# Optimization experiments

Hardware: AMD Instinct MI355X
Metric: run time of the kernel (lower is better)

Reference implementation:

```python
import jax, jax.numpy as jnp
import numpy as np

B, S, D = 1, 2048, 2048
NH, NKV, HD = 16, 8, 128
FF = 8192
L = 2
V = 32000
THETA = 10000.0
EPS = 1e-5
SCALE = 0.02


def setup_inputs() -> dict:
    key = jax.random.key(0)
    ks = jax.random.split(key, 16)
    return {
        "input_ids": jax.random.randint(ks[0], (B, S), 0, V, dtype=jnp.int32),
        "embed": jax.random.normal(ks[1], (V, D), jnp.float32) * SCALE,
        "Wq": jax.random.normal(ks[2], (L, D, NH * HD), jnp.float32) * SCALE,
        "Wk": jax.random.normal(ks[3], (L, D, NKV * HD), jnp.float32) * SCALE,
        "Wv": jax.random.normal(ks[4], (L, D, NKV * HD), jnp.float32) * SCALE,
        "Wo": jax.random.normal(ks[5], (L, NH * HD, D), jnp.float32) * SCALE,
        "Wgate": jax.random.normal(ks[6], (L, D, FF), jnp.float32) * SCALE,
        "Wup": jax.random.normal(ks[7], (L, D, FF), jnp.float32) * SCALE,
        "Wdown": jax.random.normal(ks[8], (L, FF, D), jnp.float32) * SCALE,
        "norm_attn": jnp.ones((L, D), jnp.float32),
        "norm_mlp": jnp.ones((L, D), jnp.float32),
        "norm_final": jnp.ones((D,), jnp.float32),
        "lm_head": jax.random.normal(ks[9], (D, V), jnp.float32) * SCALE,
        "D1": jax.random.normal(ks[10], (S,), jnp.float32) + 2.0,
        "D2": jax.random.normal(ks[11], (HD,), jnp.float32) + 2.0,
        "D3": jax.random.normal(ks[12], (S,), jnp.float32) + 2.0,
    }


def _rms_norm(x, w):
    return x * jax.lax.rsqrt(jnp.mean(x * x, axis=-1, keepdims=True) + EPS) * w


def _rotate_half(x):
    x1, x2 = jnp.split(x, 2, axis=-1)
    return jnp.concatenate([-x2, x1], axis=-1)


def _forward(input_ids, embed, Wq, Wk, Wv, Wo, Wgate, Wup, Wdown,
             norm_attn, norm_mlp, norm_final, lm_head, D1, D2, D3):
    # RoPE tables: [1,1,S,HD]
    inv_freq = 1.0 / (THETA ** (jnp.arange(0, HD, 2, dtype=jnp.float32) / HD))
    freqs = jnp.arange(S, dtype=jnp.float32)[:, None] * inv_freq[None, :]
    emb = jnp.concatenate([freqs, freqs], axis=-1)
    cos = jnp.cos(emb)[None, None]
    sin = jnp.sin(emb)[None, None]
    causal = jnp.tril(jnp.ones((S, S), dtype=bool))
    neg = jnp.finfo(jnp.float32).min
    D1i, D2i, D3i = 1.0 / D1, 1.0 / D2, 1.0 / D3
    n_rep = NH // NKV

    h = embed[input_ids]  # [B,S,D]
    for l in range(L):
        # --- attention block ---
        x = _rms_norm(h, norm_attn[l])
        q = (x @ Wq[l]).reshape(B, S, NH, HD).transpose(0, 2, 1, 3)   # [B,NH,S,HD]
        k = (x @ Wk[l]).reshape(B, S, NKV, HD).transpose(0, 2, 1, 3)  # [B,NKV,S,HD]
        v = (x @ Wv[l]).reshape(B, S, NKV, HD).transpose(0, 2, 1, 3)
        q = q * cos + _rotate_half(q) * sin
        k = k * cos + _rotate_half(k) * sin
        # repeat_kv (GQA)
        k = jnp.repeat(k, n_rep, axis=1)
        v = jnp.repeat(v, n_rep, axis=1)
        # TEE diagonal encryption: Q' = D1 Q D2, K'^T = D2^-1 K^T D3
        q_enc = q * D1[None, None, :, None] * D2[None, None, None, :]
        k_enc = k * D3[None, None, :, None] * D2i[None, None, None, :]
        scores = jnp.einsum('bhqd,bhkd->bhqk', q_enc, k_enc)
        # decrypt: D1^-1 (Q'K'^T) D3^-1  (mathematically cancels encryption)
        scores = scores * D1i[None, None, :, None] * D3i[None, None, None, :]
        scores = scores / jnp.sqrt(jnp.float32(HD))
        scores = jnp.where(causal[None, None], scores, neg)
        probs = jax.nn.softmax(scores, axis=-1)
        o = jnp.einsum('bhqk,bhkd->bhqd', probs, v)
        o = o.transpose(0, 2, 1, 3).reshape(B, S, NH * HD)
        h = h + o @ Wo[l]
        # --- SwiGLU MLP block ---
        x = _rms_norm(h, norm_mlp[l])
        h = h + (jax.nn.silu(x @ Wgate[l]) * (x @ Wup[l])) @ Wdown[l]

    h = _rms_norm(h, norm_final)
    return h @ lm_head  # logits [B,S,V]


def reference(input_ids, embed, Wq, Wk, Wv, Wo, Wgate, Wup, Wdown,
              norm_attn, norm_mlp, norm_final, lm_head, D1, D2, D3):
    return _forward(input_ids, embed, Wq, Wk, Wv, Wo, Wgate, Wup, Wdown,
                    norm_attn, norm_mlp, norm_final, lm_head, D1, D2, D3)
```

## Files before the change

### kernel.cpp

```cpp
#include <hip/hip_runtime.h>
#include <cstdint>
#include <cstddef>

typedef __attribute__((ext_vector_type(4))) float f32x4;
typedef __attribute__((ext_vector_type(8))) short short8;
typedef __attribute__((ext_vector_type(4))) unsigned int u32x4;

static const int TS = 2048;
static const int DM = 2048;
static const int NHEAD = 16, NKVH = 8, HDIM = 128;
static const int FFD = 8192;
static const int NVOC = 32000;
static const int QKVN = 4096;

__device__ __forceinline__ unsigned short f2bf(float f){
  unsigned int u = __builtin_bit_cast(unsigned int, f);
  u += 0x7FFFu + ((u >> 16) & 1u);
  return (unsigned short)(u >> 16);
}
__device__ __forceinline__ float bf2f(short h){
  unsigned int u = ((unsigned int)(unsigned short)h) << 16;
  return __builtin_bit_cast(float, u);
}
__device__ __forceinline__ f32x4 mfma16(short8 a, short8 b, f32x4 c){
  return __builtin_amdgcn_mfma_f32_16x16x32_bf16(a, b, c, 0, 0, 0);
}
__device__ __forceinline__ void gload16(const void* g, void* l){
  __builtin_amdgcn_global_load_lds(
      (const __attribute__((address_space(1))) unsigned int*)g,
      (__attribute__((address_space(3))) unsigned int*)l, 16, 0, 0);
}
__device__ __forceinline__ long toff(int r, int k, int ldk){
  return ((long)((r >> 4) * ldk + (k >> 5)) << 9)
       + (((k & 31) >> 3) << 7) + ((r & 15) << 3) + (k & 7);
}

__global__ void rope_tables_k(float* __restrict__ cosT, float* __restrict__ sinT){
  int idx = blockIdx.x * 256 + threadIdx.x;
  int s = idx >> 6, j = idx & 63;
  float inv = exp2f(-(float)j * (13.287712379549449f / 64.0f));
  float ang = (float)s * inv;
  cosT[idx] = cosf(ang);
  sinT[idx] = sinf(ang);
}

__global__ void embed_k(const int* __restrict__ ids, const float* __restrict__ E,
                        float* __restrict__ h){
  int s = blockIdx.x, tid = threadIdx.x;
  long id = ids[s];
  const f32x4* src = (const f32x4*)(E + id * (long)DM);
  f32x4* dst = (f32x4*)(h + (long)s * DM);
  dst[tid] = src[tid];
  dst[tid + 256] = src[tid + 256];
}

__global__ void rmsnorm_k(const float* __restrict__ x, const float* __restrict__ w,
                          short* __restrict__ out){
  int s = blockIdx.x, tid = threadIdx.x;
  const float* row = x + (long)s * DM;
  f32x4 v0 = *(const f32x4*)&row[tid * 8];
  f32x4 v1 = *(const f32x4*)&row[tid * 8 + 4];
  float ss = v0[0]*v0[0] + v0[1]*v0[1] + v0[2]*v0[2] + v0[3]*v0[3]
           + v1[0]*v1[0] + v1[1]*v1[1] + v1[2]*v1[2] + v1[3]*v1[3];
  #pragma unroll
  for (int off = 32; off; off >>= 1) ss += __shfl_xor(ss, off);
  __shared__ float sred[4];
  int wave = tid >> 6, lane = tid & 63;
  if (lane == 0) sred[wave] = ss;
  __syncthreads();
  float tot = sred[0] + sred[1] + sred[2] + sred[3];
  float r = rsqrtf(tot * (1.0f / (float)DM) + 1e-5f);
  f32x4 w0 = *(const f32x4*)&w[tid * 8];
  f32x4 w1 = *(const f32x4*)&w[tid * 8 + 4];
  short8 o;
  #pragma unroll
  for (int j = 0; j < 4; j++) o[j] = (short)f2bf(v0[j] * r * w0[j]);
  #pragma unroll
  for (int j = 0; j < 4; j++) o[4 + j] = (short)f2bf(v1[j] * r * w1[j]);
  *(short8*)&out[toff(s, tid * 8, DM >> 5)] = o;
}

__global__ void transpose_k(const float* __restrict__ B, short* __restrict__ Bt,
                            int K, int N){
  __shared__ float t[64][65];
  int tid = threadIdx.x;
  int kb = blockIdx.y * 64, nb = blockIdx.x * 64;
  int r0 = tid >> 4, c4 = tid & 15;
  const int ldk = K >> 5;
  #pragma unroll
  for (int p = 0; p < 4; p++){
    int r = r0 + p * 16;
    f32x4 v = *(const f32x4*)&B[(long)(kb + r) * N + nb + c4 * 4];
    t[r][c4*4+0] = v[0]; t[r][c4*4+1] = v[1]; t[r][c4*4+2] = v[2]; t[r][c4*4+3] = v[3];
  }
  __syncthreads();
  int n0 = tid >> 3, k0 = (tid & 7) * 8;
  #pragma unroll
  for (int p = 0; p < 2; p++){
    int n = n0 + p * 32;
    short8 o;
    #pragma unroll
    for (int j = 0; j < 8; j++) o[j] = (short)f2bf(t[k0 + j][n]);
    *(short8*)&Bt[toff(nb + n, kb + k0, ldk)] = o;
  }
}

__global__ void vtrans_k(const short* __restrict__ vb, short* __restrict__ vtb, int stride){
  int s0 = blockIdx.x * 64, kv = blockIdx.y;
  int tid = threadIdx.x;
  int s = s0 + (tid & 63);
  int d0 = (tid >> 6) * 8;
  #pragma unroll
  for (int p = 0; p < 4; p++){
    int d = d0 + p * 32;
    short8 v = *(const short8*)&vb[(long)s * stride + kv * HDIM + d];
    #pragma unroll
    for (int j = 0; j < 8; j++)
      vtb[(long)(kv * HDIM + d + j) * TS + s] = v[j];
  }
}

__global__ void rope_apply_k(short* __restrict__ buf, const float* __restrict__ cosT,
                             const float* __restrict__ sinT, int nh, int stride, int coloff){
  int idx = blockIdx.x * 256 + threadIdx.x;
  int j = idx & 63;
  int t = idx >> 6;
  int hh = t % nh;
  int s = t / nh;
  long base = (long)s * stride + coloff + hh * HDIM + j;
  float c = cosT[s * 64 + j], sn = sinT[s * 64 + j];
  float x1 = bf2f(buf[base]), x2 = bf2f(buf[base + 64]);
  buf[base]      = (short)f2bf(x1 * c - x2 * sn);
  buf[base + 64] = (short)f2bf(x2 * c + x1 * sn);
}

__global__ void reduce4_k(const float* __restrict__ p, float* __restrict__ h){
  const long stride = (long)TS * DM;
  long i = ((long)blockIdx.x * 256 + threadIdx.x) * 4;
  f32x4 a = *(const f32x4*)&h[i];
  f32x4 v0 = *(const f32x4*)&p[i];
  f32x4 v1 = *(const f32x4*)&p[i + stride];
  f32x4 v2 = *(const f32x4*)&p[i + 2 * stride];
  f32x4 v3 = *(const f32x4*)&p[i + 3 * stride];
  a = a + ((v0 + v1) + (v2 + v3));
  *(f32x4*)&h[i] = a;
}

template<int EPI>
__global__ __launch_bounds__(512, 2)
void gemm256(const short* __restrict__ A, int ldkA,
             const short* __restrict__ Bt, int ldkB,
             float* __restrict__ Cf, short* __restrict__ Cb,
             const short* __restrict__ Xtra, int N, int K, int ldkC){
  __shared__ short lds[4][2][8192];
  const int tid = threadIdx.x;
  const int wid = tid >> 6, lane = tid & 63;
  const int wr = wid >> 2, wc = wid & 3;
  const int fr = lane & 15, fch = lane >> 4;
  const int nt = K >> 5;

  const int z = blockIdx.y;
  const int k0 = z * nt;

  const int nbt = N >> 8;
  const int nwg = nbt << 3;
  const int q = nwg >> 3;
  const int swz = (blockIdx.x & 7) * q + (blockIdx.x >> 3);
  const int mb = swz & 7, nb = swz >> 3;

  const short* Abase = A  + ((long)(mb * 16) * ldkA + k0) * 512 + lane * 8;
  const short* Bbase = Bt + ((long)(nb * 16) * ldkB + k0) * 512 + lane * 8;
  const int gA0 = wid * 2, gA1 = wid * 2 + 1;

  short8 aE[4], aO[4], bE[2], bO[2];
  f32x4 acc[8][4] = {};

#define STG_A(bufc, g_, tau_) \
  gload16(Abase + ((long)(g_) * ldkA + (tau_)) * 512, &lds[bufc][0][(g_) * 512])
#define STG_B(bufc, g_, tau_) \
  gload16(Bbase + ((long)(g_) * ldkB + (tau_)) * 512, &lds[bufc][1][(g_) * 512])
#define RDA(dst, bufc, mh) do{ \
    _Pragma("unroll") \
    for (int j_ = 0; j_ < 4; j_++) \
      dst[j_] = *(const short8*)&lds[bufc][0][(wr * 8 + (mh) * 4 + j_) * 512 + fch * 128 + fr * 8]; \
  }while(0)
#define RDB(dst, bufc, nh) do{ \
    _Pragma("unroll") \
    for (int i_ = 0; i_ < 2; i_++) \
      dst[i_] = *(const short8*)&lds[bufc][1][(wc * 4 + (nh) * 2 + i_) * 512 + fch * 128 + fr * 8]; \
  }while(0)
#define MM8(va, vb, mh, nh) do{ \
    __builtin_amdgcn_s_setprio(1); \
    _Pragma("unroll") \
    for (int j_ = 0; j_ < 4; j_++) \
      _Pragma("unroll") \
      for (int i_ = 0; i_ < 2; i_++) \
        acc[(mh)*4+j_][(nh)*2+i_] = mfma16(va[j_], vb[i_], acc[(mh)*4+j_][(nh)*2+i_]); \
    __builtin_amdgcn_s_setprio(0); \
  }while(0)
#define SB __builtin_amdgcn_sched_barrier(0)

#define TILE(t_, bufR, bufN, bufS, bC, bNx) do{ \
    const int tau_ = ((t_) + 3 < nt) ? (t_) + 3 : nt - 1; \
    RDB(bNx, bufR, 1); STG_A(bufS, gA0, tau_); SB; MM8(aE, bC, 0, 0); \
    RDA(aO,  bufR, 1); STG_A(bufS, gA1, tau_); SB; MM8(aE, bNx, 0, 1); \
    asm volatile("s_waitcnt vmcnt(6)" ::: "memory"); \
    __builtin_amdgcn_s_barrier(); \
    RDA(aE,  bufN, 0); STG_B(bufS, gA0, tau_); SB; MM8(aO, bNx, 1, 1); \
    RDB(bNx, bufN, 0); STG_B(bufS, gA1, tau_); SB; MM8(aO, bC, 1, 0); \
    __builtin_amdgcn_s_barrier(); \
  }while(0)

  STG_A(0, gA0, 0); STG_A(0, gA1, 0); STG_B(0, gA0, 0); STG_B(0, gA1, 0);
  STG_A(1, gA0, 1); STG_A(1, gA1, 1); STG_B(1, gA0, 1); STG_B(1, gA1, 1);
  STG_A(2, gA0, 2); STG_A(2, gA1, 2); STG_B(2, gA0, 2); STG_B(2, gA1, 2);
  asm volatile("s_waitcnt vmcnt(8)" ::: "memory");
  __builtin_amdgcn_s_barrier();
  RDA(aE, 0, 0); RDB(bE, 0, 0);

  const int nIter = nt >> 2;
  for (int it = 0; it < nIter; ++it){
    const int t0 = it << 2;
    TILE(t0 + 0, 0, 1, 3, bE, bO);
    TILE(t0 + 1, 1, 2, 0, bO, bE);
    TILE(t0 + 2, 2, 3, 1, bE, bO);
    TILE(t0 + 3, 3, 0, 2, bO, bE);
  }
  asm volatile("s_waitcnt vmcnt(0)" ::: "memory");

#undef STG_A
#undef STG_B
#undef RDA
#undef RDB
#undef MM8
#undef SB
#undef TILE

  const int rb0 = mb * 256 + wr * 128 + fch * 4;
  const int cb0 = nb * 256 + wc * 64 + fr;
  const long pbase = (EPI == 5) ? (long)z * ((long)TS * N) : 0;
  #pragma unroll
  for (int m = 0; m < 8; m++)
    #pragma unroll
    for (int n = 0; n < 4; n++)
      #pragma unroll
      for (int i = 0; i < 4; i++){
        const int rr = rb0 + m * 16 + i, cc = cb0 + n * 16;
        long idx = (long)rr * N + cc;
        float v = acc[m][n][i];
        if constexpr (EPI == 0) Cf[idx] = v;
        else if constexpr (EPI == 1) Cb[idx] = (short)f2bf(v);
        else if constexpr (EPI == 3){
          float sg = 1.0f / (1.0f + __expf(-v));
          Cb[idx] = (short)f2bf(v * sg);
        } else if constexpr (EPI == 4){
          float g = bf2f(Xtra[idx]);
          Cb[toff(rr, cc, ldkC)] = (short)f2bf(g * v);
        } else {
          Cf[pbase + idx] = v;
        }
      }
}

__device__ __forceinline__ int qoff(int r, int cB){ return r * 256 + (cB ^ ((r & 7) << 4)); }
__device__ __forceinline__ int voff(int d, int cB){ return d * 128 + (cB ^ ((d & 7) << 4)); }
__device__ __forceinline__ int poff(int r, int cB){ return r * 128 + (cB ^ ((r & 7) << 4)); }

__global__ __launch_bounds__(256)
void attn_k(const short* __restrict__ qb, const short* __restrict__ kb,
            const short* __restrict__ vtb, short* __restrict__ ob){
  __shared__ short Qs[64 * 128];
  __shared__ short Ks[64 * 128];
  __shared__ short Vt[128 * 64];
  __shared__ short Ps[64 * 64];
  const int tid = threadIdx.x, wave = tid >> 6, lane = tid & 63;
  const int qt = blockIdx.x, head = blockIdx.y, kvh = head >> 1;
  const float scale = 0.08838834764831845f;

  {
    int r0 = tid >> 4, c16 = tid & 15;
    #pragma unroll
    for (int p = 0; p < 4; p++){
      int r = r0 + p * 16;
      u32x4 v = *(const u32x4*)&qb[(long)(qt * 64 + r) * QKVN + head * HDIM + c16 * 8];
      *(u32x4*)((char*)Qs + qoff(r, c16 * 16)) = v;
    }
  }

  float mrun[4] = {-1e30f, -1e30f, -1e30f, -1e30f};
  float lrun[4] = {0.f, 0.f, 0.f, 0.f};
  f32x4 accO[8] = {};

  for (int kt = 0; kt <= qt; kt++){
    __syncthreads();
    {
      int r0 = tid >> 4, c16 = tid & 15;
      #pragma unroll
      for (int p = 0; p < 4; p++){
        int r = r0 + p * 16;
        u32x4 v = *(const u32x4*)&kb[(long)(kt * 64 + r) * QKVN + kvh * HDIM + c16 * 8];
        *(u32x4*)((char*)Ks + qoff(r, c16 * 16)) = v;
      }
      int vr0 = tid >> 3, vc = tid & 7;
      #pragma unroll
      for (int p = 0; p < 4; p++){
        int d = vr0 + p * 32;
        u32x4 v = *(const u32x4*)&vtb[(long)(kvh * HDIM + d) * TS + kt * 64 + vc * 8];
        *(u32x4*)((char*)Vt + voff(d, vc * 16)) = v;
      }
    }
    __syncthreads();

    f32x4 sacc[4] = {};
    #pragma unroll
    for (int k4 = 0; k4 < 4; k4++){
      short8 aq = *(const short8*)((const char*)Qs +
                   qoff(wave * 16 + (lane & 15), k4 * 64 + (lane >> 4) * 16));
      #pragma unroll
      for (int n = 0; n < 4; n++){
        short8 bk = *(const short8*)((const char*)Ks +
                     qoff(n * 16 + (lane & 15), k4 * 64 + (lane >> 4) * 16));
        sacc[n] = mfma16(aq, bk, sacc[n]);
      }
    }

    const bool diag = (kt == qt);
    float mt[4] = {-1e30f, -1e30f, -1e30f, -1e30f};
    #pragma unroll
    for (int n = 0; n < 4; n++)
      #pragma unroll
      for (int i = 0; i < 4; i++){
        float v = sacc[n][i] * scale;
        if (diag){
          int rr = (lane >> 4) * 4 + i + wave * 16;
          int cc = n * 16 + (lane & 15);
          if (cc > rr) v = -1e30f;
        }
        sacc[n][i] = v;
        mt[i] = fmaxf(mt[i], v);
      }
    #pragma unroll
    for (int off = 1; off < 16; off <<= 1)
      #pragma unroll
      for (int i = 0; i < 4; i++) mt[i] = fmaxf(mt[i], __shfl_xor(mt[i], off));
    float alpha[4], rsum[4];
    #pragma unroll
    for (int i = 0; i < 4; i++){
      float mn = fmaxf(mrun[i], mt[i]);
      alpha[i] = __expf(mrun[i] - mn);
      mrun[i] = mn;
      rsum[i] = 0.f;
    }
    #pragma unroll
    for (int n = 0; n < 4; n++)
      #pragma unroll
      for (int i = 0; i < 4; i++){
        float p = __expf(sacc[n][i] - mrun[i]);
        sacc[n][i] = p;
        rsum[i] += p;
      }
    #pragma unroll
    for (int off = 1; off < 16; off <<= 1)
      #pragma unroll
      for (int i = 0; i < 4; i++) rsum[i] += __shfl_xor(rsum[i], off);
    #pragma unroll
    for (int i = 0; i < 4; i++) lrun[i] = lrun[i] * alpha[i] + rsum[i];

    #pragma unroll
    for (int n = 0; n < 4; n++)
      #pragma unroll
      for (int i = 0; i < 4; i++){
        int rr = wave * 16 + (lane >> 4) * 4 + i;
        int cc = n * 16 + (lane & 15);
        *(short*)((char*)Ps + poff(rr, cc * 2)) = (short)f2bf(sacc[n][i]);
      }

    #pragma unroll
    for (int n = 0; n < 8; n++)
      #pragma unroll
      for (int i = 0; i < 4; i++) accO[n][i] *= alpha[i];
    #pragma unroll
    for (int ks = 0; ks < 2; ks++){
      short8 ap = *(const short8*)((const char*)Ps +
                   poff(wave * 16 + (lane & 15), ks * 64 + (lane >> 4) * 16));
      #pragma unroll
      for (int n = 0; n < 8; n++){
        short8 bv = *(const short8*)((const char*)Vt +
                     voff(n * 16 + (lane & 15), ks * 64 + (lane >> 4) * 16));
        accO[n] = mfma16(ap, bv, accO[n]);
      }
    }
  }

  #pragma unroll
  for (int i = 0; i < 4; i++){
    float inv = 1.0f / lrun[i];
    int rr = qt * 64 + wave * 16 + (lane >> 4) * 4 + i;
    #pragma unroll
    for (int n = 0; n < 8; n++){
      int cc = head * HDIM + n * 16 + (lane & 15);
      ob[toff(rr, cc, DM >> 5)] = (short)f2bf(accO[n][i] * inv);
    }
  }
}

extern "C" void kernel_launch(void* const* d_in, const int* in_sizes, int n_in,
                              void* d_out, int out_size, void* d_ws, size_t ws_size,
                              hipStream_t stream){
  (void)in_sizes; (void)n_in; (void)out_size; (void)ws_size;
  const int*   ids = (const int*)d_in[0];
  const float* E   = (const float*)d_in[1];
  const float* Wq  = (const float*)d_in[2];
  const float* Wk  = (const float*)d_in[3];
  const float* Wv  = (const float*)d_in[4];
  const float* Wo  = (const float*)d_in[5];
  const float* Wg  = (const float*)d_in[6];
  const float* Wu  = (const float*)d_in[7];
  const float* Wd  = (const float*)d_in[8];
  const float* nA  = (const float*)d_in[9];
  const float* nM  = (const float*)d_in[10];
  const float* nF  = (const float*)d_in[11];
  const float* LMH = (const float*)d_in[12];
  float* out = (float*)d_out;

  char* ws = (char*)d_ws;
  size_t off = 0;
  auto alloc = [&](size_t bytes){ void* p = ws + off; off += (bytes + 255) & ~(size_t)255; return p; };
  float* h    = (float*)alloc((size_t)TS * DM * 4);
  short* xb   = (short*)alloc((size_t)TS * DM * 2);
  short* qkvb = (short*)alloc((size_t)TS * QKVN * 2);
  short* vtb  = (short*)alloc((size_t)NKVH * HDIM * TS * 2);
  short* obuf = (short*)alloc((size_t)TS * DM * 2);
  short* sg   = (short*)alloc((size_t)TS * FFD * 2);
  short* actb = (short*)alloc((size_t)TS * FFD * 2);
  float* cosT = (float*)alloc((size_t)TS * 64 * 4);
  float* sinT = (float*)alloc((size_t)TS * 64 * 4);
  short* wT   = (short*)alloc((size_t)NVOC * DM * 2);
  float* pPart = (float*)((char*)wT + (size_t)36 * 1024 * 1024);

  rope_tables_k<<<512, 256, 0, stream>>>(cosT, sinT);
  embed_k<<<TS, 256, 0, stream>>>(ids, E, h);

  for (int l = 0; l < 2; l++){
    rmsnorm_k<<<TS, 256, 0, stream>>>(h, nA + (size_t)l * DM, xb);
    transpose_k<<<dim3(32, 32), 256, 0, stream>>>(Wq + (size_t)l * DM * DM, wT, DM, DM);
    transpose_k<<<dim3(16, 32), 256, 0, stream>>>(Wk + (size_t)l * DM * 1024, wT + (size_t)2048 * DM, DM, 1024);
    transpose_k<<<dim3(16, 32), 256, 0, stream>>>(Wv + (size_t)l * DM * 1024, wT + (size_t)3072 * DM, DM, 1024);
    gemm256<1><<<dim3(128), 512, 0, stream>>>(xb, 64, wT, 64, nullptr, qkvb, nullptr, QKVN, DM, 0);
    rope_apply_k<<<8192, 256, 0, stream>>>(qkvb, cosT, sinT, NHEAD, QKVN, 0);
    rope_apply_k<<<4096, 256, 0, stream>>>(qkvb, cosT, sinT, NKVH, QKVN, 2048);
    vtrans_k<<<dim3(32, 8), 256, 0, stream>>>(qkvb + 3072, vtb, QKVN);
    attn_k<<<dim3(32, 16), 256, 0, stream>>>(qkvb, qkvb + 2048, vtb, obuf);
    transpose_k<<<dim3(32, 32), 256, 0, stream>>>(Wo + (size_t)l * DM * DM, wT, DM, DM);
    gemm256<5><<<dim3(64, 4), 512, 0, stream>>>(obuf, 64, wT, 64, pPart, nullptr, nullptr, DM, DM / 4, 0);
    reduce4_k<<<4096, 256, 0, stream>>>(pPart, h);
    rmsnorm_k<<<TS, 256, 0, stream>>>(h, nM + (size_t)l * DM, xb);
    transpose_k<<<dim3(128, 32), 256, 0, stream>>>(Wg + (size_t)l * DM * FFD, wT, DM, FFD);
    gemm256<3><<<dim3(256), 512, 0, stream>>>(xb, 64, wT, 64, nullptr, sg, nullptr, FFD, DM, 0);
    transpose_k<<<dim3(128, 32), 256, 0, stream>>>(Wu + (size_t)l * DM * FFD, wT, DM, FFD);
    gemm256<4><<<dim3(256), 512, 0, stream>>>(xb, 64, wT, 64, nullptr, actb, sg, FFD, DM, FFD >> 5);
    transpose_k<<<dim3(32, 128), 256, 0, stream>>>(Wd + (size_t)l * FFD * DM, wT, FFD, DM);
    gemm256<5><<<dim3(64, 4), 512, 0, stream>>>(actb, 256, wT, 256, pPart, nullptr, nullptr, DM, FFD / 4, 0);
    reduce4_k<<<4096, 256, 0, stream>>>(pPart, h);
  }

  rmsnorm_k<<<TS, 256, 0, stream>>>(h, nF, xb);
  transpose_k<<<dim3(500, 32), 256, 0, stream>>>(LMH, wT, DM, NVOC);
  gemm256<0><<<dim3(1000), 512, 0, stream>>>(xb, 64, wT, 64, out, nullptr, nullptr, NVOC, DM, 0);
}
```

Measured before the change: 1.359 ms.

## Fuse split-K reduction with RMSNorm and add double-buffered GEMM for LM head

Replaces the separate split-K partial reduction and following RMSNorm launches with one reduce_rms kernel that adds the partials into the residual and immediately normalizes to bf16. This drops one full pass over the residual stream per block. It also adds a new GEMM variant with two LDS buffers instead of four, using launch bounds for higher occupancy, and uses it for the large LM-head projection. The smaller LDS footprint trades pipeline depth for more resident workgroups.

```diff
diff --git a/kernel.cpp b/kernel.cpp
--- a/kernel.cpp
+++ b/kernel.cpp
@@ -77,6 +77,49 @@
   for (int j = 0; j < 4; j++) o[j] = (short)f2bf(v0[j] * r * w0[j]);
   #pragma unroll
   for (int j = 0; j < 4; j++) o[4 + j] = (short)f2bf(v1[j] * r * w1[j]);
+  *(short8*)&out[toff(s, tid * 8, DM >> 5)] = o;
+}
+
+__global__ void reduce_rms_k(const float* __restrict__ p, float* __restrict__ h,
+                             const float* __restrict__ w, short* __restrict__ out){
+  const long stride = (long)TS * DM;
+  int s = blockIdx.x, tid = threadIdx.x;
+  long i = (long)s * DM + tid * 8;
+  f32x4 a0 = *(const f32x4*)&h[i];
+  f32x4 a1 = *(const f32x4*)&h[i + 4];
+  {
+    f32x4 v0 = *(const f32x4*)&p[i];
+    f32x4 v1 = *(const f32x4*)&p[i + stride];
+    f32x4 v2 = *(const f32x4*)&p[i + 2 * stride];
+    f32x4 v3 = *(const f32x4*)&p[i + 3 * stride];
+    a0 = a0 + ((v0 + v1) + (v2 + v3));
+  }
+  {
+    f32x4 v0 = *(const f32x4*)&p[i + 4];
+    f32x4 v1 = *(const f32x4*)&p[i + 4 + stride];
+    f32x4 v2 = *(const f32x4*)&p[i + 4 + 2 * stride];
+    f32x4 v3 = *(const f32x4*)&p[i + 4 + 3 * stride];
+    a1 = a1 + ((v0 + v1) + (v2 + v3));
+  }
+  *(f32x4*)&h[i] = a0;
+  *(f32x4*)&h[i + 4] = a1;
+  float ss = a0[0]*a0[0] + a0[1]*a0[1] + a0[2]*a0[2] + a0[3]*a0[3]
+           + a1[0]*a1[0] + a1[1]*a1[1] + a1[2]*a1[2] + a1[3]*a1[3];
+  #pragma unroll
+  for (int off = 32; off; off >>= 1) ss += __shfl_xor(ss, off);
+  __shared__ float sred[4];
+  int wave = tid >> 6, lane = tid & 63;
+  if (lane == 0) sred[wave] = ss;
+  __syncthreads();
+  float tot = sred[0] + sred[1] + sred[2] + sred[3];
+  float r = rsqrtf(tot * (1.0f / (float)DM) + 1e-5f);
+  f32x4 w0 = *(const f32x4*)&w[tid * 8];
+  f32x4 w1 = *(const f32x4*)&w[tid * 8 + 4];
+  short8 o;
+  #pragma unroll
+  for (int j = 0; j < 4; j++) o[j] = (short)f2bf(a0[j] * r * w0[j]);
+  #pragma unroll
+  for (int j = 0; j < 4; j++) o[4 + j] = (short)f2bf(a1[j] * r * w1[j]);
   *(short8*)&out[toff(s, tid * 8, DM >> 5)] = o;
 }
 
@@ -132,18 +175,6 @@
   float x1 = bf2f(buf[base]), x2 = bf2f(buf[base + 64]);
   buf[base]      = (short)f2bf(x1 * c - x2 * sn);
   buf[base + 64] = (short)f2bf(x2 * c + x1 * sn);
-}
-
-__global__ void reduce4_k(const float* __restrict__ p, float* __restrict__ h){
-  const long stride = (long)TS * DM;
-  long i = ((long)blockIdx.x * 256 + threadIdx.x) * 4;
-  f32x4 a = *(const f32x4*)&h[i];
-  f32x4 v0 = *(const f32x4*)&p[i];
-  f32x4 v1 = *(const f32x4*)&p[i + stride];
-  f32x4 v2 = *(const f32x4*)&p[i + 2 * stride];
-  f32x4 v3 = *(const f32x4*)&p[i + 3 * stride];
-  a = a + ((v0 + v1) + (v2 + v3));
-  *(f32x4*)&h[i] = a;
 }
 
 template<int EPI>
@@ -258,6 +289,112 @@
           Cb[toff(rr, cc, ldkC)] = (short)f2bf(g * v);
         } else {
           Cf[pbase + idx] = v;
+        }
+      }
+}
+
+template<int EPI>
+__global__ __launch_bounds__(512, 4)
+void gemm256_2b(const short* __restrict__ A, int ldkA,
+                const short* __restrict__ Bt, int ldkB,
+                float* __restrict__ Cf, short* __restrict__ Cb,
+                const short* __restrict__ Xtra, int N, int K, int ldkC){
+  __shared__ short lds[2][2][8192];
+  const int tid = threadIdx.x;
+  const int wid = tid >> 6, lane = tid & 63;
+  const int wr = wid >> 2, wc = wid & 3;
+  const int fr = lane & 15, fch = lane >> 4;
+  const int nt = K >> 5;
+
+  const int nbt = N >> 8;
+  const int nwg = nbt << 3;
+  const int q = nwg >> 3;
+  const int swz = (blockIdx.x & 7) * q + (blockIdx.x >> 3);
+  const int mb = swz & 7, nb = swz >> 3;
+
+  const short* Abase = A  + (long)(mb * 16) * ldkA * 512 + lane * 8;
+  const short* Bbase = Bt + (long)(nb * 16) * ldkB * 512 + lane * 8;
+  const int gA0 = wid * 2, gA1 = wid * 2 + 1;
+
+  short8 aE[4], aO[4], bE[2], bO[2];
+  f32x4 acc[8][4] = {};
+
+#define STG_A(bufc, g_, tau_) \
+  gload16(Abase + ((long)(g_) * ldkA + (tau_)) * 512, &lds[bufc][0][(g_) * 512])
+#define STG_B(bufc, g_, tau_) \
+  gload16(Bbase + ((long)(g_) * ldkB + (tau_)) * 512, &lds[bufc][1][(g_) * 512])
+#define RDA(dst, bufc, mh) do{ \
+    _Pragma("unroll") \
+    for (int j_ = 0; j_ < 4; j_++) \
+      dst[j_] = *(const short8*)&lds[bufc][0][(wr * 8 + (mh) * 4 + j_) * 512 + fch * 128 + fr * 8]; \
+  }while(0)
+#define RDB(dst, bufc, nh) do{ \
+    _Pragma("unroll") \
+    for (int i_ = 0; i_ < 2; i_++) \
+      dst[i_] = *(const short8*)&lds[bufc][1][(wc * 4 + (nh) * 2 + i_) * 512 + fch * 128 + fr * 8]; \
+  }while(0)
+#define MM8(va, vb, mh, nh) do{ \
+    __builtin_amdgcn_s_setprio(1); \
+    _Pragma("unroll") \
+    for (int j_ = 0; j_ < 4; j_++) \
+      _Pragma("unroll") \
+      for (int i_ = 0; i_ < 2; i_++) \
+        acc[(mh)*4+j_][(nh)*2+i_] = mfma16(va[j_], vb[i_], acc[(mh)*4+j_][(nh)*2+i_]); \
+    __builtin_amdgcn_s_setprio(0); \
+  }while(0)
+#define SB __builtin_amdgcn_sched_barrier(0)
+
+#define TILE2(t_, bufR, bufS) do{ \
+    if ((t_) + 1 < nt){ \
+      STG_A(bufS, gA0, (t_) + 1); STG_A(bufS, gA1, (t_) + 1); \
+      STG_B(bufS, gA0, (t_) + 1); STG_B(bufS, gA1, (t_) + 1); \
+    } \
+    RDA(aE, bufR, 0); RDB(bE, bufR, 0); \
+    RDB(bO, bufR, 1); SB; MM8(aE, bE, 0, 0); \
+    RDA(aO, bufR, 1); SB; MM8(aE, bO, 0, 1); \
+    SB; MM8(aO, bO, 1, 1); MM8(aO, bE, 1, 0); \
+    asm volatile("s_waitcnt vmcnt(0)" ::: "memory"); \
+    __builtin_amdgcn_s_barrier(); \
+  }while(0)
+
+  STG_A(0, gA0, 0); STG_A(0, gA1, 0); STG_B(0, gA0, 0); STG_B(0, gA1, 0);
+  asm volatile("s_waitcnt vmcnt(0)" ::: "memory");
+  __builtin_amdgcn_s_barrier();
+
+  const int nIter = nt >> 1;
+  for (int it = 0; it < nIter; ++it){
+    const int t0 = it << 1;
+    TILE2(t0 + 0, 0, 1);
+    TILE2(t0 + 1, 1, 0);
+  }
+
+#undef STG_A
+#undef STG_B
+#undef RDA
+#undef RDB
+#undef MM8
+#undef SB
+#undef TILE2
+
+  const int rb0 = mb * 256 + wr * 128 + fch * 4;
+  const int cb0 = nb * 256 + wc * 64 + fr;
+  #pragma unroll
+  for (int m = 0; m < 8; m++)
+    #pragma unroll
+    for (int n = 0; n < 4; n++)
+      #pragma unroll
+      for (int i = 0; i < 4; i++){
+        const int rr = rb0 + m * 16 + i, cc = cb0 + n * 16;
+        long idx = (long)rr * N + cc;
+        float v = acc[m][n][i];
+        if constexpr (EPI == 0) Cf[idx] = v;
+        else if constexpr (EPI == 1) Cb[idx] = (short)f2bf(v);
+        else if constexpr (EPI == 3){
+          float sg = 1.0f / (1.0f + __expf(-v));
+          Cb[idx] = (short)f2bf(v * sg);
+        } else if constexpr (EPI == 4){
+          float g = bf2f(Xtra[idx]);
+          Cb[toff(rr, cc, ldkC)] = (short)f2bf(g * v);
         }
       }
 }
@@ -440,9 +577,9 @@
 
   rope_tables_k<<<512, 256, 0, stream>>>(cosT, sinT);
   embed_k<<<TS, 256, 0, stream>>>(ids, E, h);
+  rmsnorm_k<<<TS, 256, 0, stream>>>(h, nA, xb);
 
   for (int l = 0; l < 2; l++){
-    rmsnorm_k<<<TS, 256, 0, stream>>>(h, nA + (size_t)l * DM, xb);
     transpose_k<<<dim3(32, 32), 256, 0, stream>>>(Wq + (size_t)l * DM * DM, wT, DM, DM);
     transpose_k<<<dim3(16, 32), 256, 0, stream>>>(Wk + (size_t)l * DM * 1024, wT + (size_t)2048 * DM, DM, 1024);
     transpose_k<<<dim3(16, 32), 256, 0, stream>>>(Wv + (size_t)l * DM * 1024, wT + (size_t)3072 * DM, DM, 1024);
@@ -453,18 +590,19 @@
     attn_k<<<dim3(32, 16), 256, 0, stream>>>(qkvb, qkvb + 2048, vtb, obuf);
     transpose_k<<<dim3(32, 32), 256, 0, stream>>>(Wo + (size_t)l * DM * DM, wT, DM, DM);
     gemm256<5><<<dim3(64, 4), 512, 0, stream>>>(obuf, 64, wT, 64, pPart, nullptr, nullptr, DM, DM / 4, 0);
-    reduce4_k<<<4096, 256, 0, stream>>>(pPart, h);
-    rmsnorm_k<<<TS, 256, 0, stream>>>(h, nM + (size_t)l * DM, xb);
+    reduce_rms_k<<<TS, 256, 0, stream>>>(pPart, h, nM + (size_t)l * DM, xb);
     transpose_k<<<dim3(128, 32), 256, 0, stream>>>(Wg + (size_t)l * DM * FFD, wT, DM, FFD);
     gemm256<3><<<dim3(256), 512, 0, stream>>>(xb, 64, wT, 64, nullptr, sg, nullptr, FFD, DM, 0);
     transpose_k<<<dim3(128, 32), 256, 0, stream>>>(Wu + (size_t)l * DM * FFD, wT, DM, FFD);
     gemm256<4><<<dim3(256), 512, 0, stream>>>(xb, 64, wT, 64, nullptr, actb, sg, FFD, DM, FFD >> 5);
     transpose_k<<<dim3(32, 128), 256, 0, stream>>>(Wd + (size_t)l * FFD * DM, wT, FFD, DM);
     gemm256<5><<<dim3(64, 4), 512, 0, stream>>>(actb, 256, wT, 256, pPart, nullptr, nullptr, DM, FFD / 4, 0);
-    reduce4_k<<<4096, 256, 0, stream>>>(pPart, h);
-  }
-
-  rmsnorm_k<<<TS, 256, 0, stream>>>(h, nF, xb);
+    if (l == 0)
+      reduce_rms_k<<<TS, 256, 0, stream>>>(pPart, h, nA + (size_t)DM, xb);
+    else
+      reduce_rms_k<<<TS, 256, 0, stream>>>(pPart, h, nF, xb);
+  }
+
   transpose_k<<<dim3(500, 32), 256, 0, stream>>>(LMH, wT, DM, NVOC);
-  gemm256<0><<<dim3(1000), 512, 0, stream>>>(xb, 64, wT, 64, out, nullptr, nullptr, NVOC, DM, 0);
-}
+  gemm256_2b<0><<<dim3(1000), 512, 0, stream>>>(xb, 64, wT, 64, out, nullptr, nullptr, NVOC, DM, 0);
+}
```

New measurement: 3.912 ms. +187.9%, slower.
